# Kernel optimization log

Measured on AMD Instinct MI355X. Metric: run time of the kernel, lower is better.

The kernel has to match this reference:

```python
import jax, jax.numpy as jnp
import numpy as np

N = 50000      # nodes
E = 800000     # edges (before self loops)
D = 128        # input_dim == hidden_dim == out_channels
H = 1          # heads
L = 3          # layers
SLOPE = 0.2    # GATv2 leaky_relu negative slope


def setup_inputs() -> dict:
    key = jax.random.key(0)
    ks = jax.random.split(key, 9)
    x = jax.random.normal(ks[0], (N, D), dtype=jnp.float32)
    edge_index = jax.random.randint(ks[1], (2, E), 0, N, dtype=jnp.int32)
    s = 1.0 / np.sqrt(D).astype(np.float32)
    # stacked per-layer GATv2Conv params (all layers are D -> H*D here)
    Wl = jax.random.normal(ks[2], (L, D, H * D), dtype=jnp.float32) * s   # lin_l weights
    bl = jnp.zeros((L, H * D), dtype=jnp.float32)
    Wr = jax.random.normal(ks[3], (L, D, H * D), dtype=jnp.float32) * s   # lin_r weights
    br = jnp.zeros((L, H * D), dtype=jnp.float32)
    att = jax.random.normal(ks[4], (L, H, D), dtype=jnp.float32) * s      # attention vector
    bias = jnp.zeros((L, H * D), dtype=jnp.float32)                       # conv output bias
    return {"x": x, "edge_index": edge_index, "Wl": Wl, "bl": bl,
            "Wr": Wr, "br": br, "att": att, "bias": bias}


def reference(x, edge_index, Wl, bl, Wr, br, att, bias):
    # add self loops (PyG GATv2Conv default)
    loops = jnp.arange(N, dtype=edge_index.dtype)
    src = jnp.concatenate([edge_index[0], loops])  # [E+N] message sources j
    dst = jnp.concatenate([edge_index[1], loops])  # [E+N] message targets i

    h = x
    for l in range(L):
        xl = (h @ Wl[l] + bl[l]).reshape(N, H, D)   # source transform
        xr = (h @ Wr[l] + br[l]).reshape(N, H, D)   # target transform
        # edge-wise GATv2 score: att . leaky_relu(xl_j + xr_i)
        e = jax.nn.leaky_relu(xl[src] + xr[dst], SLOPE)      # [E+N, H, D]
        score = jnp.einsum('ehd,hd->eh', e, att[l])          # [E+N, H]
        # segment softmax over incoming edges of each dst node
        m = jax.ops.segment_max(score, dst, num_segments=N)  # [N, H]
        p = jnp.exp(score - m[dst])
        denom = jax.ops.segment_sum(p, dst, num_segments=N)
        alpha = p / (denom[dst] + 1e-16)                     # [E+N, H]
        # weighted scatter-aggregate of source features
        msg = xl[src] * alpha[:, :, None]                    # [E+N, H, D]
        h = jax.ops.segment_sum(msg, dst, num_segments=N).reshape(N, H * D) + bias[l]
        h = jax.nn.relu(h)
    return jax.nn.log_softmax(h, axis=1)
```

## Files before the change

### kernel.cpp

```cpp
#include <hip/hip_runtime.h>
#include <cstdint>
#include <cstddef>

#define N_NODES 50000
#define N_EDGES 800000
#define ET (N_EDGES + N_NODES)
#define D 128
#define NLAYERS 3
#define SLOPE 0.2f
#define NB_SCAN ((N_NODES + 1023) / 1024)
#define GEMM_BLOCKS (((N_NODES + 127) / 128) * 2)
#define EDGE_BLOCKS ((ET + 255) / 256)

typedef __bf16 bf16x8 __attribute__((ext_vector_type(8)));
typedef float  f32x4  __attribute__((ext_vector_type(4)));
typedef float  f32x2  __attribute__((ext_vector_type(2)));

__device__ __forceinline__ unsigned short f2bf_rne(float v) {
    unsigned u = __float_as_uint(v);
    u += 0x7fffu + ((u >> 16) & 1u);
    return (unsigned short)(u >> 16);
}
__device__ __forceinline__ float bf2f(unsigned short h) {
    return __uint_as_float(((unsigned)h) << 16);
}
__device__ __forceinline__ f32x2 unpack_bf2(unsigned u) {
    f32x2 r;
    r.x = __uint_as_float(u << 16);
    r.y = __uint_as_float(u & 0xffff0000u);
    return r;
}

__global__ void prep_kernel(const float* __restrict__ x,
                            const float* __restrict__ Wl,
                            const float* __restrict__ Wr,
                            const int* __restrict__ dstp,
                            unsigned short* __restrict__ hhi,
                            unsigned short* __restrict__ hlo,
                            unsigned short* __restrict__ wlh,
                            unsigned short* __restrict__ wll,
                            unsigned short* __restrict__ wrh,
                            int* __restrict__ deg)
{
    int idx = blockIdx.x * blockDim.x + threadIdx.x;
    if (idx < (N_NODES * D) / 4) {
        float4 v = ((const float4*)x)[idx];
        unsigned short h0 = f2bf_rne(v.x), h1 = f2bf_rne(v.y);
        unsigned short h2 = f2bf_rne(v.z), h3 = f2bf_rne(v.w);
        unsigned short l0 = f2bf_rne(v.x - bf2f(h0)), l1 = f2bf_rne(v.y - bf2f(h1));
        unsigned short l2 = f2bf_rne(v.z - bf2f(h2)), l3 = f2bf_rne(v.w - bf2f(h3));
        uint2 hw, lw;
        hw.x = (unsigned)h0 | ((unsigned)h1 << 16);
        hw.y = (unsigned)h2 | ((unsigned)h3 << 16);
        lw.x = (unsigned)l0 | ((unsigned)l1 << 16);
        lw.y = (unsigned)l2 | ((unsigned)l3 << 16);
        ((uint2*)hhi)[idx] = hw;
        ((uint2*)hlo)[idx] = lw;
    }
    if (idx < NLAYERS * D * D) {
        int l   = idx / (D * D);
        int rem = idx - l * D * D;
        int kk  = rem / D;
        int nn  = rem - kk * D;
        int tp  = l * D * D + nn * D + kk;
        float v = Wl[idx];
        unsigned short h = f2bf_rne(v);
        wlh[tp] = h;
        wll[tp] = f2bf_rne(v - bf2f(h));
        wrh[tp] = f2bf_rne(Wr[idx]);
    }
    if (idx < ET) {
        int dt = (idx < N_EDGES) ? dstp[idx] : idx - N_EDGES;
        atomicAdd(deg + dt, 1);
    }
}

__global__ void scan1_kernel(const int* __restrict__ deg,
                             int* __restrict__ incl, int* __restrict__ bsum)
{
    __shared__ int tmp[1024];
    int tid = threadIdx.x;
    int i = blockIdx.x * 1024 + tid;
    int v = (i < N_NODES) ? deg[i] : 0;
    tmp[tid] = v;
    __syncthreads();
    #pragma unroll
    for (int o = 1; o < 1024; o <<= 1) {
        int t = (tid >= o) ? tmp[tid - o] : 0;
        __syncthreads();
        tmp[tid] += t;
        __syncthreads();
    }
    if (i < N_NODES) incl[i] = tmp[tid];
    if (tid == 1023) bsum[blockIdx.x] = tmp[1023];
}

__global__ void scan3_kernel(const int* __restrict__ deg, const int* __restrict__ incl,
                             const int* __restrict__ bsum,
                             int* __restrict__ off, int* __restrict__ cursor)
{
    __shared__ int sb[NB_SCAN + 1];
    int tid = threadIdx.x;
    if (tid < 64) {
        int v = (tid < NB_SCAN) ? bsum[tid] : 0;
        int orig = v;
        #pragma unroll
        for (int o = 1; o < 64; o <<= 1) {
            int t = __shfl_up(v, o, 64);
            if (tid >= o) v += t;
        }
        if (tid < NB_SCAN) sb[tid] = v - orig;
        if (tid == 63)     sb[NB_SCAN] = v;
    }
    __syncthreads();
    int i = blockIdx.x * blockDim.x + tid;
    if (i < N_NODES) {
        int e = incl[i] - deg[i] + sb[i >> 10];
        off[i] = e;
        cursor[i] = e;
    } else if (i == N_NODES) {
        off[N_NODES] = sb[NB_SCAN];
    }
}

template <bool WITH_SCATTER>
__global__ __launch_bounds__(256, 2)
void gemm_mfma_kernel(const unsigned short* __restrict__ hhi,
                      const unsigned short* __restrict__ hlo,
                      const unsigned short* __restrict__ wlh,
                      const unsigned short* __restrict__ wll,
                      const unsigned short* __restrict__ wrh,
                      const float* __restrict__ bl, const float* __restrict__ br,
                      const float* __restrict__ att,
                      unsigned short* __restrict__ xlb, unsigned short* __restrict__ xrb,
                      float* __restrict__ bs,
                      const int* __restrict__ srcp, const int* __restrict__ dstp,
                      int* __restrict__ cursor, int* __restrict__ esrc, int n)
{
    if (WITH_SCATTER && blockIdx.x >= GEMM_BLOCKS) {
        int e = (blockIdx.x - GEMM_BLOCKS) * 256 + threadIdx.x;
        if (e < ET) {
            int s, dt;
            if (e < N_EDGES) { s = srcp[e]; dt = dstp[e]; }
            else             { s = e - N_EDGES; dt = s; }
            int pos = atomicAdd(cursor + dt, 1);
            esrc[pos] = s;
        }
        return;
    }

    int lane = threadIdx.x & 63;
    int wid  = threadIdx.x >> 6;
    int rowB = blockIdx.x >> 1;
    int c0   = (blockIdx.x & 1) * 64;
    int m0   = (rowB * 4 + wid) * 32;
    if (m0 >= n) return;
    int gl = lane & 15;
    int kg = lane >> 4;

    float blc[4], brc[4], attc[4];
    #pragma unroll
    for (int t = 0; t < 4; t++) {
        blc[t]  = bl [c0 + t * 16 + gl];
        brc[t]  = br [c0 + t * 16 + gl];
        attc[t] = att[c0 + t * 16 + gl];
    }

    int ar0 = m0 + gl;      if (ar0 >= n) ar0 = n - 1;
    int ar1 = m0 + 16 + gl; if (ar1 >= n) ar1 = n - 1;
    const unsigned short* ah0 = hhi + (size_t)ar0 * D + kg * 8;
    const unsigned short* al0 = hlo + (size_t)ar0 * D + kg * 8;
    const unsigned short* ah1 = hhi + (size_t)ar1 * D + kg * 8;
    const unsigned short* al1 = hlo + (size_t)ar1 * D + kg * 8;

    f32x4 accl[2][4], accr[2][4];
    #pragma unroll
    for (int rt = 0; rt < 2; rt++)
        #pragma unroll
        for (int t = 0; t < 4; t++) {
            accl[rt][t] = (f32x4){0.f, 0.f, 0.f, 0.f};
            accr[rt][t] = (f32x4){0.f, 0.f, 0.f, 0.f};
        }

    #pragma unroll
    for (int ks = 0; ks < 4; ks++) {
        bf16x8 aH0 = *(const bf16x8*)(ah0 + ks * 32);
        bf16x8 aL0 = *(const bf16x8*)(al0 + ks * 32);
        bf16x8 aH1 = *(const bf16x8*)(ah1 + ks * 32);
        bf16x8 aL1 = *(const bf16x8*)(al1 + ks * 32);
        #pragma unroll
        for (int t = 0; t < 4; t++) {
            size_t boff = (size_t)(c0 + t * 16 + gl) * D + kg * 8 + ks * 32;
            bf16x8 bLH = *(const bf16x8*)(wlh + boff);
            bf16x8 bLL = *(const bf16x8*)(wll + boff);
            bf16x8 bRH = *(const bf16x8*)(wrh + boff);
            accl[0][t] = __builtin_amdgcn_mfma_f32_16x16x32_bf16(aH0, bLH, accl[0][t], 0, 0, 0);
            accl[0][t] = __builtin_amdgcn_mfma_f32_16x16x32_bf16(aL0, bLH, accl[0][t], 0, 0, 0);
            accl[0][t] = __builtin_amdgcn_mfma_f32_16x16x32_bf16(aH0, bLL, accl[0][t], 0, 0, 0);
            accr[0][t] = __builtin_amdgcn_mfma_f32_16x16x32_bf16(aH0, bRH, accr[0][t], 0, 0, 0);
            accl[1][t] = __builtin_amdgcn_mfma_f32_16x16x32_bf16(aH1, bLH, accl[1][t], 0, 0, 0);
            accl[1][t] = __builtin_amdgcn_mfma_f32_16x16x32_bf16(aL1, bLH, accl[1][t], 0, 0, 0);
            accl[1][t] = __builtin_amdgcn_mfma_f32_16x16x32_bf16(aH1, bLL, accl[1][t], 0, 0, 0);
            accr[1][t] = __builtin_amdgcn_mfma_f32_16x16x32_bf16(aH1, bRH, accr[1][t], 0, 0, 0);
        }
    }

    #pragma unroll
    for (int rt = 0; rt < 2; rt++) {
        #pragma unroll
        for (int r = 0; r < 4; r++) {
            int row = m0 + rt * 16 + kg * 4 + r;
            if (row < n) {
                float p = 0.f;
                #pragma unroll
                for (int t = 0; t < 4; t++) {
                    int col = c0 + t * 16 + gl;
                    float vl = accl[rt][t][r] + blc[t];
                    xlb[(size_t)row * D + col] = f2bf_rne(vl);
                    xrb[(size_t)row * D + col] = f2bf_rne(accr[rt][t][r] + brc[t]);
                    p = fmaf(attc[t], vl, p);
                }
                p += __shfl_xor(p, 1, 64);
                p += __shfl_xor(p, 2, 64);
                p += __shfl_xor(p, 4, 64);
                p += __shfl_xor(p, 8, 64);
                if (gl == 0) unsafeAtomicAdd(bs + row, 0.6f * p);
            }
        }
    }
}

template <int LAST>
__global__ void node_attn_kernel(const unsigned short* __restrict__ xlb,
                                 const unsigned short* __restrict__ xrb,
                                 const float* __restrict__ bs,
                                 const float* __restrict__ att,
                                 const float* __restrict__ bias,
                                 const int* __restrict__ off,
                                 const int* __restrict__ esrc,
                                 float* __restrict__ outF,
                                 unsigned short* __restrict__ hhi,
                                 unsigned short* __restrict__ hlo)
{
    int i    = (int)((blockIdx.x * (size_t)blockDim.x + threadIdx.x) >> 6);
    int lane = threadIdx.x & 63;
    if (i >= N_NODES) return;
    int g  = lane >> 4;
    int gl = lane & 15;
    int fb = gl * 8;

    float aav[8], rrv[8];
    {
        float4 a0 = *(const float4*)(att + fb);
        float4 a1 = *(const float4*)(att + fb + 4);
        aav[0] = 0.4f * a0.x; aav[1] = 0.4f * a0.y; aav[2] = 0.4f * a0.z; aav[3] = 0.4f * a0.w;
        aav[4] = 0.4f * a1.x; aav[5] = 0.4f * a1.y; aav[6] = 0.4f * a1.z; aav[7] = 0.4f * a1.w;
        uint4 r4 = *(const uint4*)(xrb + (size_t)i * D + fb);
        f32x2 q;
        q = unpack_bf2(r4.x); rrv[0] = q.x; rrv[1] = q.y;
        q = unpack_bf2(r4.y); rrv[2] = q.x; rrv[3] = q.y;
        q = unpack_bf2(r4.z); rrv[4] = q.x; rrv[5] = q.y;
        q = unpack_bf2(r4.w); rrv[6] = q.x; rrv[7] = q.y;
    }

    float m = -1e30f, l = 0.f;
    float acc[8];
    #pragma unroll
    for (int j = 0; j < 8; j++) acc[j] = 0.f;

    int k    = off[i];
    int kEnd = off[i + 1];
    int last = kEnd - 1;

    int ka = k + g, kb = k + 4 + g;
    bool va = ka < kEnd, vb = kb < kEnd;
    int sa = esrc[va ? ka : last];
    int sb = esrc[vb ? kb : last];
    uint4 x4a = *(const uint4*)(xlb + (size_t)sa * D + fb);
    uint4 x4b = *(const uint4*)(xlb + (size_t)sb * D + fb);
    float bsa = bs[sa], bsb = bs[sb];

    while (k < kEnd) {
        int kn = k + 8;
        uint4 nxa = x4a, nxb = x4b;
        float nbsa = bsa, nbsb = bsb;
        bool nva = false, nvb = false;
        if (kn < kEnd) {
            int nka = kn + g, nkb = kn + 4 + g;
            nva = nka < kEnd; nvb = nkb < kEnd;
            int nsa = esrc[nva ? nka : last];
            int nsb = esrc[nvb ? nkb : last];
            nxa = *(const uint4*)(xlb + (size_t)nsa * D + fb);
            nxb = *(const uint4*)(xlb + (size_t)nsb * D + fb);
            nbsa = bs[nsa]; nbsb = bs[nsb];
        }
        float xa[8], xb[8];
        {
            f32x2 q;
            q = unpack_bf2(x4a.x); xa[0] = q.x; xa[1] = q.y;
            q = unpack_bf2(x4a.y); xa[2] = q.x; xa[3] = q.y;
            q = unpack_bf2(x4a.z); xa[4] = q.x; xa[5] = q.y;
            q = unpack_bf2(x4a.w); xa[6] = q.x; xa[7] = q.y;
            q = unpack_bf2(x4b.x); xb[0] = q.x; xb[1] = q.y;
            q = unpack_bf2(x4b.y); xb[2] = q.x; xb[3] = q.y;
            q = unpack_bf2(x4b.z); xb[4] = q.x; xb[5] = q.y;
            q = unpack_bf2(x4b.w); xb[6] = q.x; xb[7] = q.y;
        }
        float s2a = 0.f, s2b = 0.f;
        #pragma unroll
        for (int j = 0; j < 8; j++) {
            s2a = fmaf(aav[j], fabsf(xa[j] + rrv[j]), s2a);
            s2b = fmaf(aav[j], fabsf(xb[j] + rrv[j]), s2b);
        }
        s2a += __shfl_xor(s2a, 1, 64);
        s2b += __shfl_xor(s2b, 1, 64);
        s2a += __shfl_xor(s2a, 2, 64);
        s2b += __shfl_xor(s2b, 2, 64);
        s2a += __shfl_xor(s2a, 4, 64);
        s2b += __shfl_xor(s2b, 4, 64);
        s2a += __shfl_xor(s2a, 8, 64);
        s2b += __shfl_xor(s2b, 8, 64);
        float sca = bsa + s2a;
        float scb = bsb + s2b;
        float mx2 = fmaxf(sca, scb);
        if (__any(mx2 > m + 8.f)) {
            float mn = fmaxf(m, mx2);
            float f  = __expf(m - mn);
            float pa = va ? __expf(sca - mn) : 0.f;
            float pb = vb ? __expf(scb - mn) : 0.f;
            l = l * f + pa + pb;
            #pragma unroll
            for (int j = 0; j < 8; j++)
                acc[j] = fmaf(acc[j], f, fmaf(xa[j], pa, xb[j] * pb));
            m = mn;
        } else {
            float pa = va ? __expf(sca - m) : 0.f;
            float pb = vb ? __expf(scb - m) : 0.f;
            l += pa + pb;
            #pragma unroll
            for (int j = 0; j < 8; j++)
                acc[j] = fmaf(xa[j], pa, fmaf(xb[j], pb, acc[j]));
        }
        x4a = nxa; x4b = nxb; bsa = nbsa; bsb = nbsb; va = nva; vb = nvb;
        k = kn;
    }

    #pragma unroll
    for (int o = 16; o <= 32; o <<= 1) {
        float mo  = __shfl_xor(m, o, 64);
        float lo2 = __shfl_xor(l, o, 64);
        float mn  = fmaxf(m, mo);
        float f1  = __expf(m - mn);
        float f2s = __expf(mo - mn);
        l = l * f1 + lo2 * f2s;
        #pragma unroll
        for (int j = 0; j < 8; j++) {
            float ao = __shfl_xor(acc[j], o, 64);
            acc[j] = acc[j] * f1 + ao * f2s;
        }
        m = mn;
    }

    float inv = 1.f / (l + 1e-16f);
    float hv[8];
    {
        float4 b0 = *(const float4*)(bias + fb);
        float4 b1 = *(const float4*)(bias + fb + 4);
        float bb[8] = {b0.x, b0.y, b0.z, b0.w, b1.x, b1.y, b1.z, b1.w};
        #pragma unroll
        for (int j = 0; j < 8; j++) hv[j] = fmaxf(fmaf(acc[j], inv, bb[j]), 0.f);
    }

    if (LAST) {
        float mx = hv[0];
        #pragma unroll
        for (int j = 1; j < 8; j++) mx = fmaxf(mx, hv[j]);
        mx = fmaxf(mx, __shfl_xor(mx, 1, 64));
        mx = fmaxf(mx, __shfl_xor(mx, 2, 64));
        mx = fmaxf(mx, __shfl_xor(mx, 4, 64));
        mx = fmaxf(mx, __shfl_xor(mx, 8, 64));
        float se = 0.f;
        #pragma unroll
        for (int j = 0; j < 8; j++) se += __expf(hv[j] - mx);
        se += __shfl_xor(se, 1, 64);
        se += __shfl_xor(se, 2, 64);
        se += __shfl_xor(se, 4, 64);
        se += __shfl_xor(se, 8, 64);
        float ls = logf(se) + mx;
        if (g == 0) {
            float4 o0 = make_float4(hv[0] - ls, hv[1] - ls, hv[2] - ls, hv[3] - ls);
            float4 o1 = make_float4(hv[4] - ls, hv[5] - ls, hv[6] - ls, hv[7] - ls);
            float* dst = outF + (size_t)i * D + fb;
            *(float4*)(dst)     = o0;
            *(float4*)(dst + 4) = o1;
        }
    } else {
        if (g < 2) {
            unsigned pk[4];
            #pragma unroll
            for (int j = 0; j < 4; j++) {
                float v0 = hv[j * 2], v1 = hv[j * 2 + 1];
                unsigned short h0 = f2bf_rne(v0), h1 = f2bf_rne(v1);
                if (g == 0) pk[j] = (unsigned)h0 | ((unsigned)h1 << 16);
                else {
                    unsigned short l0 = f2bf_rne(v0 - bf2f(h0));
                    unsigned short l1 = f2bf_rne(v1 - bf2f(h1));
                    pk[j] = (unsigned)l0 | ((unsigned)l1 << 16);
                }
            }
            unsigned short* dst = (g == 0 ? hhi : hlo) + (size_t)i * D + fb;
            *(uint4*)dst = make_uint4(pk[0], pk[1], pk[2], pk[3]);
        }
    }
}

extern "C" void kernel_launch(void* const* d_in, const int* in_sizes, int n_in,
                              void* d_out, int out_size, void* d_ws, size_t ws_size,
                              hipStream_t stream)
{
    const float* x    = (const float*)d_in[0];
    const int*   ei   = (const int*)  d_in[1];
    const float* Wl   = (const float*)d_in[2];
    const float* bl   = (const float*)d_in[3];
    const float* Wr   = (const float*)d_in[4];
    const float* br   = (const float*)d_in[5];
    const float* att  = (const float*)d_in[6];
    const float* bias = (const float*)d_in[7];
    float* out = (float*)d_out;

    const int* srcp = ei;
    const int* dstp = ei + N_EDGES;

    const size_t ND = (size_t)N_NODES * D;
    const size_t WSZ = (size_t)NLAYERS * D * D;
    char* ws = (char*)d_ws;
    unsigned short* xlb = (unsigned short*)ws; ws += ND * sizeof(unsigned short);
    unsigned short* xrb = (unsigned short*)ws; ws += ND * sizeof(unsigned short);
    unsigned short* hhi = (unsigned short*)ws; ws += ND * sizeof(unsigned short);
    unsigned short* hlo = (unsigned short*)ws; ws += ND * sizeof(unsigned short);
    unsigned short* wlh = (unsigned short*)ws; ws += WSZ * sizeof(unsigned short);
    unsigned short* wll = (unsigned short*)ws; ws += WSZ * sizeof(unsigned short);
    unsigned short* wrh = (unsigned short*)ws; ws += WSZ * sizeof(unsigned short);
    float* bs   = (float*)ws; ws += (size_t)N_NODES * sizeof(float);
    int* deg    = (int*)ws;  ws += (size_t)N_NODES * sizeof(int);
    int* incl   = (int*)ws;  ws += (size_t)N_NODES * sizeof(int);
    int* off    = (int*)ws;  ws += (size_t)(N_NODES + 1) * sizeof(int);
    int* cursor = (int*)ws;  ws += (size_t)N_NODES * sizeof(int);
    int* bsum   = (int*)ws;  ws += (size_t)NB_SCAN * sizeof(int);
    int* esrc   = (int*)ws;  ws += (size_t)ET * sizeof(int);

    const int prepGrid  = (int)((ND / 4 + 255) / 256);
    const int nodeGrid  = (N_NODES + 3) / 4;
    const int scan3Grid = (N_NODES + 1 + 255) / 256;

    hipMemsetAsync(deg, 0, (size_t)N_NODES * sizeof(int), stream);
    prep_kernel<<<prepGrid, 256, 0, stream>>>(x, Wl, Wr, dstp,
                                              hhi, hlo, wlh, wll, wrh, deg);

    scan1_kernel<<<NB_SCAN, 1024, 0, stream>>>(deg, incl, bsum);
    scan3_kernel<<<scan3Grid, 256, 0, stream>>>(deg, incl, bsum, off, cursor);

    for (int l = 0; l < NLAYERS; l++) {
        size_t wOff = (size_t)l * D * D;
        hipMemsetAsync(bs, 0, (size_t)N_NODES * sizeof(float), stream);
        if (l == 0) {
            gemm_mfma_kernel<true><<<GEMM_BLOCKS + EDGE_BLOCKS, 256, 0, stream>>>(
                hhi, hlo, wlh + wOff, wll + wOff, wrh + wOff,
                bl + (size_t)l * D, br + (size_t)l * D, att + (size_t)l * D,
                xlb, xrb, bs, srcp, dstp, cursor, esrc, N_NODES);
        } else {
            gemm_mfma_kernel<false><<<GEMM_BLOCKS, 256, 0, stream>>>(
                hhi, hlo, wlh + wOff, wll + wOff, wrh + wOff,
                bl + (size_t)l * D, br + (size_t)l * D, att + (size_t)l * D,
                xlb, xrb, bs, nullptr, nullptr, nullptr, nullptr, N_NODES);
        }

        if (l == NLAYERS - 1) {
            node_attn_kernel<1><<<nodeGrid, 256, 0, stream>>>(
                xlb, xrb, bs, att + (size_t)l * D, bias + (size_t)l * D,
                off, esrc, out, nullptr, nullptr);
        } else {
            node_attn_kernel<0><<<nodeGrid, 256, 0, stream>>>(
                xlb, xrb, bs, att + (size_t)l * D, bias + (size_t)l * D,
                off, esrc, nullptr, hhi, hlo);
        }
    }
}
```

Measured before the change: 338.7 us.

## Drop split-bf16 GEMM precision, use exp2 softmax and plain per-half score stores

```diff
diff --git a/kernel.cpp b/kernel.cpp
--- a/kernel.cpp
+++ b/kernel.cpp
@@ -8,6 +8,8 @@
 #define D 128
 #define NLAYERS 3
 #define SLOPE 0.2f
+#define LOG2E 1.44269504f
+#define DEFER_THR 11.5415603f
 #define NB_SCAN ((N_NODES + 1023) / 1024)
 #define GEMM_BLOCKS (((N_NODES + 127) / 128) * 2)
 #define EDGE_BLOCKS ((ET + 255) / 256)
@@ -20,9 +22,6 @@
     unsigned u = __float_as_uint(v);
     u += 0x7fffu + ((u >> 16) & 1u);
     return (unsigned short)(u >> 16);
-}
-__device__ __forceinline__ float bf2f(unsigned short h) {
-    return __uint_as_float(((unsigned)h) << 16);
 }
 __device__ __forceinline__ f32x2 unpack_bf2(unsigned u) {
     f32x2 r;
@@ -36,26 +35,17 @@
                             const float* __restrict__ Wr,
                             const int* __restrict__ dstp,
                             unsigned short* __restrict__ hhi,
-                            unsigned short* __restrict__ hlo,
                             unsigned short* __restrict__ wlh,
-                            unsigned short* __restrict__ wll,
                             unsigned short* __restrict__ wrh,
                             int* __restrict__ deg)
 {
     int idx = blockIdx.x * blockDim.x + threadIdx.x;
     if (idx < (N_NODES * D) / 4) {
         float4 v = ((const float4*)x)[idx];
-        unsigned short h0 = f2bf_rne(v.x), h1 = f2bf_rne(v.y);
-        unsigned short h2 = f2bf_rne(v.z), h3 = f2bf_rne(v.w);
-        unsigned short l0 = f2bf_rne(v.x - bf2f(h0)), l1 = f2bf_rne(v.y - bf2f(h1));
-        unsigned short l2 = f2bf_rne(v.z - bf2f(h2)), l3 = f2bf_rne(v.w - bf2f(h3));
-        uint2 hw, lw;
-        hw.x = (unsigned)h0 | ((unsigned)h1 << 16);
-        hw.y = (unsigned)h2 | ((unsigned)h3 << 16);
-        lw.x = (unsigned)l0 | ((unsigned)l1 << 16);
-        lw.y = (unsigned)l2 | ((unsigned)l3 << 16);
+        uint2 hw;
+        hw.x = (unsigned)f2bf_rne(v.x) | ((unsigned)f2bf_rne(v.y) << 16);
+        hw.y = (unsigned)f2bf_rne(v.z) | ((unsigned)f2bf_rne(v.w) << 16);
         ((uint2*)hhi)[idx] = hw;
-        ((uint2*)hlo)[idx] = lw;
     }
     if (idx < NLAYERS * D * D) {
         int l   = idx / (D * D);
@@ -63,10 +53,7 @@
         int kk  = rem / D;
         int nn  = rem - kk * D;
         int tp  = l * D * D + nn * D + kk;
-        float v = Wl[idx];
-        unsigned short h = f2bf_rne(v);
-        wlh[tp] = h;
-        wll[tp] = f2bf_rne(v - bf2f(h));
+        wlh[tp] = f2bf_rne(Wl[idx]);
         wrh[tp] = f2bf_rne(Wr[idx]);
     }
     if (idx < ET) {
@@ -97,7 +84,8 @@
 
 __global__ void scan3_kernel(const int* __restrict__ deg, const int* __restrict__ incl,
                              const int* __restrict__ bsum,
-                             int* __restrict__ off, int* __restrict__ cursor)
+                             int* __restrict__ off, int* __restrict__ cursor,
+                             int* __restrict__ esrc)
 {
     __shared__ int sb[NB_SCAN + 1];
     int tid = threadIdx.x;
@@ -113,6 +101,7 @@
         if (tid == 63)     sb[NB_SCAN] = v;
     }
     __syncthreads();
+    if (blockIdx.x == 0 && tid < 16) esrc[ET + tid] = 0;
     int i = blockIdx.x * blockDim.x + tid;
     if (i < N_NODES) {
         int e = incl[i] - deg[i] + sb[i >> 10];
@@ -126,14 +115,12 @@
 template <bool WITH_SCATTER>
 __global__ __launch_bounds__(256, 2)
 void gemm_mfma_kernel(const unsigned short* __restrict__ hhi,
-                      const unsigned short* __restrict__ hlo,
                       const unsigned short* __restrict__ wlh,
-                      const unsigned short* __restrict__ wll,
                       const unsigned short* __restrict__ wrh,
                       const float* __restrict__ bl, const float* __restrict__ br,
                       const float* __restrict__ att,
                       unsigned short* __restrict__ xlb, unsigned short* __restrict__ xrb,
-                      float* __restrict__ bs,
+                      float* __restrict__ bs2,
                       const int* __restrict__ srcp, const int* __restrict__ dstp,
                       int* __restrict__ cursor, int* __restrict__ esrc, int n)
 {
@@ -152,7 +139,8 @@
     int lane = threadIdx.x & 63;
     int wid  = threadIdx.x >> 6;
     int rowB = blockIdx.x >> 1;
-    int c0   = (blockIdx.x & 1) * 64;
+    int half = blockIdx.x & 1;
+    int c0   = half * 64;
     int m0   = (rowB * 4 + wid) * 32;
     if (m0 >= n) return;
     int gl = lane & 15;
@@ -169,9 +157,14 @@
     int ar0 = m0 + gl;      if (ar0 >= n) ar0 = n - 1;
     int ar1 = m0 + 16 + gl; if (ar1 >= n) ar1 = n - 1;
     const unsigned short* ah0 = hhi + (size_t)ar0 * D + kg * 8;
-    const unsigned short* al0 = hlo + (size_t)ar0 * D + kg * 8;
     const unsigned short* ah1 = hhi + (size_t)ar1 * D + kg * 8;
-    const unsigned short* al1 = hlo + (size_t)ar1 * D + kg * 8;
+
+    bf16x8 Ah0[4], Ah1[4];
+    #pragma unroll
+    for (int ks = 0; ks < 4; ks++) {
+        Ah0[ks] = *(const bf16x8*)(ah0 + ks * 32);
+        Ah1[ks] = *(const bf16x8*)(ah1 + ks * 32);
+    }
 
     f32x4 accl[2][4], accr[2][4];
     #pragma unroll
@@ -184,24 +177,15 @@
 
     #pragma unroll
     for (int ks = 0; ks < 4; ks++) {
-        bf16x8 aH0 = *(const bf16x8*)(ah0 + ks * 32);
-        bf16x8 aL0 = *(const bf16x8*)(al0 + ks * 32);
-        bf16x8 aH1 = *(const bf16x8*)(ah1 + ks * 32);
-        bf16x8 aL1 = *(const bf16x8*)(al1 + ks * 32);
         #pragma unroll
         for (int t = 0; t < 4; t++) {
             size_t boff = (size_t)(c0 + t * 16 + gl) * D + kg * 8 + ks * 32;
             bf16x8 bLH = *(const bf16x8*)(wlh + boff);
-            bf16x8 bLL = *(const bf16x8*)(wll + boff);
             bf16x8 bRH = *(const bf16x8*)(wrh + boff);
-            accl[0][t] = __builtin_amdgcn_mfma_f32_16x16x32_bf16(aH0, bLH, accl[0][t], 0, 0, 0);
-            accl[0][t] = __builtin_amdgcn_mfma_f32_16x16x32_bf16(aL0, bLH, accl[0][t], 0, 0, 0);
-            accl[0][t] = __builtin_amdgcn_mfma_f32_16x16x32_bf16(aH0, bLL, accl[0][t], 0, 0, 0);
-            accr[0][t] = __builtin_amdgcn_mfma_f32_16x16x32_bf16(aH0, bRH, accr[0][t], 0, 0, 0);
-            accl[1][t] = __builtin_amdgcn_mfma_f32_16x16x32_bf16(aH1, bLH, accl[1][t], 0, 0, 0);
-            accl[1][t] = __builtin_amdgcn_mfma_f32_16x16x32_bf16(aL1, bLH, accl[1][t], 0, 0, 0);
-            accl[1][t] = __builtin_amdgcn_mfma_f32_16x16x32_bf16(aH1, bLL, accl[1][t], 0, 0, 0);
-            accr[1][t] = __builtin_amdgcn_mfma_f32_16x16x32_bf16(aH1, bRH, accr[1][t], 0, 0, 0);
+            accl[0][t] = __builtin_amdgcn_mfma_f32_16x16x32_bf16(Ah0[ks], bLH, accl[0][t], 0, 0, 0);
+            accr[0][t] = __builtin_amdgcn_mfma_f32_16x16x32_bf16(Ah0[ks], bRH, accr[0][t], 0, 0, 0);
+            accl[1][t] = __builtin_amdgcn_mfma_f32_16x16x32_bf16(Ah1[ks], bLH, accl[1][t], 0, 0, 0);
+            accr[1][t] = __builtin_amdgcn_mfma_f32_16x16x32_bf16(Ah1[ks], bRH, accr[1][t], 0, 0, 0);
         }
     }
 
@@ -224,7 +208,7 @@
                 p += __shfl_xor(p, 2, 64);
                 p += __shfl_xor(p, 4, 64);
                 p += __shfl_xor(p, 8, 64);
-                if (gl == 0) unsafeAtomicAdd(bs + row, 0.6f * p);
+                if (gl == 0) bs2[row * 2 + half] = 0.6f * LOG2E * p;
             }
         }
     }
@@ -233,14 +217,13 @@
 template <int LAST>
 __global__ void node_attn_kernel(const unsigned short* __restrict__ xlb,
                                  const unsigned short* __restrict__ xrb,
-                                 const float* __restrict__ bs,
+                                 const float* __restrict__ bs2,
                                  const float* __restrict__ att,
                                  const float* __restrict__ bias,
                                  const int* __restrict__ off,
                                  const int* __restrict__ esrc,
                                  float* __restrict__ outF,
-                                 unsigned short* __restrict__ hhi,
-                                 unsigned short* __restrict__ hlo)
+                                 unsigned short* __restrict__ hhi)
 {
     int i    = (int)((blockIdx.x * (size_t)blockDim.x + threadIdx.x) >> 6);
     int lane = threadIdx.x & 63;
@@ -253,8 +236,9 @@
     {
         float4 a0 = *(const float4*)(att + fb);
         float4 a1 = *(const float4*)(att + fb + 4);
-        aav[0] = 0.4f * a0.x; aav[1] = 0.4f * a0.y; aav[2] = 0.4f * a0.z; aav[3] = 0.4f * a0.w;
-        aav[4] = 0.4f * a1.x; aav[5] = 0.4f * a1.y; aav[6] = 0.4f * a1.z; aav[7] = 0.4f * a1.w;
+        const float s = 0.4f * LOG2E;
+        aav[0] = s * a0.x; aav[1] = s * a0.y; aav[2] = s * a0.z; aav[3] = s * a0.w;
+        aav[4] = s * a1.x; aav[5] = s * a1.y; aav[6] = s * a1.z; aav[7] = s * a1.w;
         uint4 r4 = *(const uint4*)(xrb + (size_t)i * D + fb);
         f32x2 q;
         q = unpack_bf2(r4.x); rrv[0] = q.x; rrv[1] = q.y;
@@ -270,15 +254,16 @@
 
     int k    = off[i];
     int kEnd = off[i + 1];
-    int last = kEnd - 1;
 
     int ka = k + g, kb = k + 4 + g;
     bool va = ka < kEnd, vb = kb < kEnd;
-    int sa = esrc[va ? ka : last];
-    int sb = esrc[vb ? kb : last];
+    int sa = esrc[ka];
+    int sb = esrc[kb];
     uint4 x4a = *(const uint4*)(xlb + (size_t)sa * D + fb);
     uint4 x4b = *(const uint4*)(xlb + (size_t)sb * D + fb);
-    float bsa = bs[sa], bsb = bs[sb];
+    float2 ba2 = *(const float2*)(bs2 + sa * 2);
+    float2 bb2 = *(const float2*)(bs2 + sb * 2);
+    float bsa = ba2.x + ba2.y, bsb = bb2.x + bb2.y;
 
     while (k < kEnd) {
         int kn = k + 8;
@@ -288,11 +273,13 @@
         if (kn < kEnd) {
             int nka = kn + g, nkb = kn + 4 + g;
             nva = nka < kEnd; nvb = nkb < kEnd;
-            int nsa = esrc[nva ? nka : last];
-            int nsb = esrc[nvb ? nkb : last];
+            int nsa = esrc[nka];
+            int nsb = esrc[nkb];
             nxa = *(const uint4*)(xlb + (size_t)nsa * D + fb);
             nxb = *(const uint4*)(xlb + (size_t)nsb * D + fb);
-            nbsa = bs[nsa]; nbsb = bs[nsb];
+            float2 na2 = *(const float2*)(bs2 + nsa * 2);
+            float2 nb2 = *(const float2*)(bs2 + nsb * 2);
+            nbsa = na2.x + na2.y; nbsb = nb2.x + nb2.y;
         }
         float xa[8], xb[8];
         {
@@ -323,19 +310,19 @@
         float sca = bsa + s2a;
         float scb = bsb + s2b;
         float mx2 = fmaxf(sca, scb);
-        if (__any(mx2 > m + 8.f)) {
+        if (__any(mx2 > m + DEFER_THR)) {
             float mn = fmaxf(m, mx2);
-            float f  = __expf(m - mn);
-            float pa = va ? __expf(sca - mn) : 0.f;
-            float pb = vb ? __expf(scb - mn) : 0.f;
+            float f  = exp2f(m - mn);
+            float pa = va ? exp2f(sca - mn) : 0.f;
+            float pb = vb ? exp2f(scb - mn) : 0.f;
             l = l * f + pa + pb;
             #pragma unroll
             for (int j = 0; j < 8; j++)
                 acc[j] = fmaf(acc[j], f, fmaf(xa[j], pa, xb[j] * pb));
             m = mn;
         } else {
-            float pa = va ? __expf(sca - m) : 0.f;
-            float pb = vb ? __expf(scb - m) : 0.f;
+            float pa = va ? exp2f(sca - m) : 0.f;
+            float pb = vb ? exp2f(scb - m) : 0.f;
             l += pa + pb;
             #pragma unroll
             for (int j = 0; j < 8; j++)
@@ -350,8 +337,8 @@
         float mo  = __shfl_xor(m, o, 64);
         float lo2 = __shfl_xor(l, o, 64);
         float mn  = fmaxf(m, mo);
-        float f1  = __expf(m - mn);
-        float f2s = __expf(mo - mn);
+        float f1  = exp2f(m - mn);
+        float f2s = exp2f(mo - mn);
         l = l * f1 + lo2 * f2s;
         #pragma unroll
         for (int j = 0; j < 8; j++) {
@@ -395,20 +382,14 @@
             *(float4*)(dst + 4) = o1;
         }
     } else {
-        if (g < 2) {
+        if (g == 0) {
             unsigned pk[4];
             #pragma unroll
             for (int j = 0; j < 4; j++) {
-                float v0 = hv[j * 2], v1 = hv[j * 2 + 1];
-                unsigned short h0 = f2bf_rne(v0), h1 = f2bf_rne(v1);
-                if (g == 0) pk[j] = (unsigned)h0 | ((unsigned)h1 << 16);
-                else {
-                    unsigned short l0 = f2bf_rne(v0 - bf2f(h0));
-                    unsigned short l1 = f2bf_rne(v1 - bf2f(h1));
-                    pk[j] = (unsigned)l0 | ((unsigned)l1 << 16);
-                }
+                pk[j] = (unsigned)f2bf_rne(hv[j * 2]) |
+                        ((unsigned)f2bf_rne(hv[j * 2 + 1]) << 16);
             }
-            unsigned short* dst = (g == 0 ? hhi : hlo) + (size_t)i * D + fb;
+            unsigned short* dst = hhi + (size_t)i * D + fb;
             *(uint4*)dst = make_uint4(pk[0], pk[1], pk[2], pk[3]);
         }
     }
@@ -437,52 +418,48 @@
     unsigned short* xlb = (unsigned short*)ws; ws += ND * sizeof(unsigned short);
     unsigned short* xrb = (unsigned short*)ws; ws += ND * sizeof(unsigned short);
     unsigned short* hhi = (unsigned short*)ws; ws += ND * sizeof(unsigned short);
-    unsigned short* hlo = (unsigned short*)ws; ws += ND * sizeof(unsigned short);
     unsigned short* wlh = (unsigned short*)ws; ws += WSZ * sizeof(unsigned short);
-    unsigned short* wll = (unsigned short*)ws; ws += WSZ * sizeof(unsigned short);
     unsigned short* wrh = (unsigned short*)ws; ws += WSZ * sizeof(unsigned short);
-    float* bs   = (float*)ws; ws += (size_t)N_NODES * sizeof(float);
+    float* bs2  = (float*)ws; ws += (size_t)N_NODES * 2 * sizeof(float);
     int* deg    = (int*)ws;  ws += (size_t)N_NODES * sizeof(int);
     int* incl   = (int*)ws;  ws += (size_t)N_NODES * sizeof(int);
     int* off    = (int*)ws;  ws += (size_t)(N_NODES + 1) * sizeof(int);
     int* cursor = (int*)ws;  ws += (size_t)N_NODES * sizeof(int);
     int* bsum   = (int*)ws;  ws += (size_t)NB_SCAN * sizeof(int);
-    int* esrc   = (int*)ws;  ws += (size_t)ET * sizeof(int);
+    int* esrc   = (int*)ws;  ws += ((size_t)ET + 16) * sizeof(int);
 
     const int prepGrid  = (int)((ND / 4 + 255) / 256);
     const int nodeGrid  = (N_NODES + 3) / 4;
     const int scan3Grid = (N_NODES + 1 + 255) / 256;
 
     hipMemsetAsync(deg, 0, (size_t)N_NODES * sizeof(int), stream);
-    prep_kernel<<<prepGrid, 256, 0, stream>>>(x, Wl, Wr, dstp,
-                                              hhi, hlo, wlh, wll, wrh, deg);
+    prep_kernel<<<prepGrid, 256, 0, stream>>>(x, Wl, Wr, dstp, hhi, wlh, wrh, deg);
 
     scan1_kernel<<<NB_SCAN, 1024, 0, stream>>>(deg, incl, bsum);
-    scan3_kernel<<<scan3Grid, 256, 0, stream>>>(deg, incl, bsum, off, cursor);
+    scan3_kernel<<<scan3Grid, 256, 0, stream>>>(deg, incl, bsum, off, cursor, esrc);
 
     for (int l = 0; l < NLAYERS; l++) {
         size_t wOff = (size_t)l * D * D;
-        hipMemsetAsync(bs, 0, (size_t)N_NODES * sizeof(float), stream);
         if (l == 0) {
             gemm_mfma_kernel<true><<<GEMM_BLOCKS + EDGE_BLOCKS, 256, 0, stream>>>(
-                hhi, hlo, wlh + wOff, wll + wOff, wrh + wOff,
+                hhi, wlh + wOff, wrh + wOff,
                 bl + (size_t)l * D, br + (size_t)l * D, att + (size_t)l * D,
-                xlb, xrb, bs, srcp, dstp, cursor, esrc, N_NODES);
+                xlb, xrb, bs2, srcp, dstp, cursor, esrc, N_NODES);
         } else {
             gemm_mfma_kernel<false><<<GEMM_BLOCKS, 256, 0, stream>>>(
-                hhi, hlo, wlh + wOff, wll + wOff, wrh + wOff,
+                hhi, wlh + wOff, wrh + wOff,
                 bl + (size_t)l * D, br + (size_t)l * D, att + (size_t)l * D,
-                xlb, xrb, bs, nullptr, nullptr, nullptr, nullptr, N_NODES);
+                xlb, xrb, bs2, nullptr, nullptr, nullptr, nullptr, N_NODES);
         }
 
         if (l == NLAYERS - 1) {
             node_attn_kernel<1><<<nodeGrid, 256, 0, stream>>>(
-                xlb, xrb, bs, att + (size_t)l * D, bias + (size_t)l * D,
-                off, esrc, out, nullptr, nullptr);
+                xlb, xrb, bs2, att + (size_t)l * D, bias + (size_t)l * D,
+                off, esrc, out, nullptr);
         } else {
             node_attn_kernel<0><<<nodeGrid, 256, 0, stream>>>(
-                xlb, xrb, bs, att + (size_t)l * D, bias + (size_t)l * D,
-                off, esrc, nullptr, hhi, hlo);
-        }
-    }
-}
+                xlb, xrb, bs2, att + (size_t)l * D, bias + (size_t)l * D,
+                off, esrc, nullptr, hhi);
+        }
+    }
+}
```

Result: no change. 332.5 us (-1.8%).
